# Optimization experiments

Measured on AMD Instinct MI355X. Metric: run time of the kernel, lower is better.

The kernel has to match this reference:

```python
import jax, jax.numpy as jnp
import numpy as np

B, H, W_LEN = 16, 256, 4096          # batch, height (in channels), width
R, S, L, NC = 128, 256, 16, 12       # residual ch, skip ch, n_layers, n_classes
MAX_DILATION = 256
LOOP = int(np.floor(np.log2(MAX_DILATION))) + 1  # 9 -> dilations 1..256 cycling


def conv1d(x, w, b=None, dilation=1):
    # x: [N, C, T], w: [O, I, K]
    y = jax.lax.conv_general_dilated(
        x, w, window_strides=(1,), padding='VALID',
        rhs_dilation=(dilation,), dimension_numbers=('NCH', 'OIH', 'NCH'))
    return y if b is None else y + b[None, :, None]


def setup_inputs() -> dict:
    key = jax.random.key(0)
    ks = jax.random.split(key, 8)
    f = lambda k, sh: (jax.random.normal(k, sh, jnp.float32) * 0.05)
    return {
        'input_data': jax.random.normal(ks[0], (B, H, W_LEN), jnp.float32),
        'w_in': f(ks[1], (R, H, 1)),         'b_in': jnp.zeros((R,), jnp.float32),
        'dilate_w': f(ks[2], (L, 2 * R, R, 2)), 'dilate_b': jnp.zeros((L, 2 * R), jnp.float32),
        'res_w': f(ks[3], (L - 1, R, R, 1)), 'res_b': jnp.zeros((L - 1, R), jnp.float32),
        'skip_w': f(ks[4], (L, S, R, 1)),    'skip_b': jnp.zeros((L, S), jnp.float32),
        'w_out': f(ks[5], (NC, S, 1)),
        'lin_w': f(ks[6], (NC, NC)),         'lin_b': jnp.zeros((NC,), jnp.float32),
    }


def reference(input_data, w_in, b_in, dilate_w, dilate_b, res_w, res_b,
              skip_w, skip_b, w_out, lin_w, lin_b):
    x = conv1d(input_data, w_in, b_in)   # [B, R, T]
    res_acts = None
    skip = None
    for i in range(L):
        d = 2 ** (i % LOOP)
        xi = jnp.pad(x, ((0, 0), (0, 0), (d, 0)))  # causal pad (k-1)*d, k=2
        a = conv1d(xi, dilate_w[i], dilate_b[i], dilation=d)  # [B, 2R, T]
        acts = jnp.tanh(a[:, :R]) * jax.nn.sigmoid(a[:, R:])
        if i < L - 1:
            res_acts = conv1d(acts, res_w[i], res_b[i])
        # NOTE: faithful to original: last layer reuses previous res_acts
        x = res_acts + x
        sk = conv1d(acts, skip_w[i], skip_b[i])
        skip = sk if i == 0 else skip + sk
    out = conv1d(skip, w_out)            # [B, NC, T], no bias
    out = jnp.mean(out, axis=2)          # AvgPool1d(kernel=W_LEN) + view -> [B, NC]
    return out @ lin_w.T + lin_b
```

## Files before the change

### kernel.cpp

```cpp
#include <hip/hip_runtime.h>
#include <hip/hip_bf16.h>


#define KC 32

typedef __bf16 bf16_t;
typedef __bf16 bf16x4 __attribute__((ext_vector_type(4)));
typedef __bf16 bf16x8 __attribute__((ext_vector_type(8)));
typedef float f32x16 __attribute__((ext_vector_type(16)));

__device__ __align__(16) __bf16 g_wi_dev[32768];
__device__ float g_pooled[4096];

__device__ __forceinline__ void gl_lds16(const void* g, void* l) {
    __builtin_amdgcn_global_load_lds(
        (const __attribute__((address_space(1))) unsigned int*)g,
        (__attribute__((address_space(3))) unsigned int*)l, 16, 0, 0);
}

__device__ __forceinline__ float fast_sigmoid(float x) {
    float e = __builtin_amdgcn_exp2f(-1.4426950408889634f * x);
    return __builtin_amdgcn_rcpf(1.0f + e);
}
__device__ __forceinline__ float fast_tanh(float x) {
    float e = __builtin_amdgcn_exp2f(-2.8853900817779268f * x);
    return fmaf(2.0f, __builtin_amdgcn_rcpf(1.0f + e), -1.0f);
}

__global__ __launch_bounds__(256) void prep_wg_kernel(
    const float* __restrict__ dw, bf16_t* __restrict__ wg)
{
    int idx = blockIdx.x * 256 + threadIdx.x;
    int e = idx & 7, ps = (idx >> 3) & 3, row = (idx >> 5) & 255;
    int c = (idx >> 13) & 7, layer = idx >> 16;
    int s = ps ^ ((row >> 1) & 3);
    int k = c * 32 + s * 8 + e;
    int tap = k >> 7, ch = k & 127;
    wg[idx] = (bf16_t)dw[(((size_t)layer * 256 + row) * 128 + ch) * 2 + tap];
}

__global__ __launch_bounds__(256) void prep_wr_kernel(
    const float* __restrict__ rw, bf16_t* __restrict__ wr)
{
    int idx = blockIdx.x * 256 + threadIdx.x;
    int e = idx & 7, ps = (idx >> 3) & 3, row = (idx >> 5) & 127;
    int c = (idx >> 12) & 3, layer = idx >> 14;
    int s = ps ^ ((row >> 1) & 3);
    int ch = c * 32 + s * 8 + e;
    wr[idx] = (bf16_t)rw[((size_t)layer * 128 + row) * 128 + ch];
}

__global__ __launch_bounds__(256) void prep_wi_kernel(const float* __restrict__ wi)
{
    int idx = blockIdx.x * 256 + threadIdx.x;
    int e = idx & 7, ps = (idx >> 3) & 3, row = (idx >> 5) & 127;
    int c = idx >> 12;
    int s = ps ^ ((row >> 1) & 3);
    int ch = c * 32 + s * 8 + e;
    g_wi_dev[idx] = (bf16_t)wi[(size_t)row * 256 + ch];
}

__global__ __launch_bounds__(256) void zero_misc_kernel(bf16_t* __restrict__ zeros)
{
    int idx = blockIdx.x * 256 + threadIdx.x;
    zeros[idx] = (bf16_t)0.0f;
    if (idx < 4096) g_pooled[idx] = 0.0f;
}

__global__ __launch_bounds__(256) void transpose_in(
    const float* __restrict__ input, bf16_t* __restrict__ th,
    bf16_t* __restrict__ tl, int b_off)
{
    __shared__ float Sl[64][65];
    const int tid = threadIdx.x;
    const int t0 = blockIdx.x * 64, ch0 = blockIdx.y * 64, bz = blockIdx.z;
    const int b = b_off + bz;
#pragma unroll
    for (int it = 0; it < 16; ++it) {
        int idx = it * 256 + tid;
        int t = idx & 63, ch = idx >> 6;
        Sl[ch][t] = input[((size_t)b * 256 + ch0 + ch) * 4096 + t0 + t];
    }
    __syncthreads();
#pragma unroll
    for (int it = 0; it < 16; ++it) {
        int idx = it * 256 + tid;
        int ch = idx & 63, t = idx >> 6;
        float v = Sl[ch][t];
        bf16_t hb = (bf16_t)v;
        size_t o = ((size_t)bz * 4096 + t0 + t) * 256 + ch0 + ch;
        th[o] = hb;
        tl[o] = (bf16_t)(v - (float)hb);
    }
}

__global__ __launch_bounds__(512, 4) void fused_layer(
    const bf16_t* __restrict__ xc_hi, const bf16_t* __restrict__ xc_lo,
    bf16_t* __restrict__ xn_hi, bf16_t* __restrict__ xn_lo,
    const bf16_t* __restrict__ zeros,
    const bf16_t* __restrict__ wg_l, const float* __restrict__ dbias,
    const bf16_t* __restrict__ wr_l, const float* __restrict__ rbias,
    float* __restrict__ asum_l, int d, int skipres)
{
    __shared__ __align__(16) char lds[66560];
    const int tid = threadIdx.x;
    const int wave = tid >> 6, lane = tid & 63;
    const int l31 = lane & 31, h = lane >> 5;
    const int wm = wave & 3, wn = wave >> 2;

    const int wg = blockIdx.x + 32 * blockIdx.z;
    const int xcd = wg & 7;
    const int idxin = wg >> 3;
    const int b = (xcd << 1) | (idxin >> 5);
    const int tile = idxin & 31;
    const int t0 = tile * 128;

    f32x16 acc[2][2];
#pragma unroll
    for (int m = 0; m < 2; ++m)
#pragma unroll
        for (int n = 0; n < 2; ++n) acc[m][n] = (f32x16)(0.0f);

    const int t_pos = tid >> 2;
    const int s_x = (tid & 3) ^ ((t_pos >> 1) & 3);
    const int chx = s_x << 3;

    auto stage_g = [&](int u, int sl) {
        const char* wsrc = (const char*)wg_l + (size_t)u * 16384;
        char* wdst = lds + sl * 16384;
        gl_lds16(wsrc + tid * 16, wdst + tid * 16);
        gl_lds16(wsrc + (tid + 512) * 16, wdst + (tid + 512) * 16);
        int tap = (u >> 2) & 1;
        int ch = ((u & 3) << 5) + chx;
        int tg = t0 + t_pos - (tap ? 0 : d);
        const bf16_t* sph = (tg >= 0)
            ? (xc_hi + ((size_t)b * 4096 + tg) * 128 + ch) : (zeros + ch);
        gl_lds16(sph, lds + 32768 + sl * 8192 + tid * 16);
    };

    stage_g(0, 0);
    const int swz = (l31 >> 1) & 3;
    int aoff[2][2], boff[2][2];
#pragma unroll
    for (int m = 0; m < 2; ++m)
#pragma unroll
        for (int s2 = 0; s2 < 2; ++s2)
            aoff[m][s2] = ((m ? 128 + wm * 32 : wm * 32) + l31) * 64 +
                          (((s2 * 2 + h) ^ swz) << 4);
#pragma unroll
    for (int n = 0; n < 2; ++n)
#pragma unroll
        for (int s2 = 0; s2 < 2; ++s2)
            boff[n][s2] = (wn * 64 + n * 32 + l31) * 64 + (((s2 * 2 + h) ^ swz) << 4);

    for (int u = 0; u < 8; ++u) {
        if (u < 7) {
            stage_g(u + 1, (u + 1) & 1);
            asm volatile("s_waitcnt vmcnt(3)" ::: "memory");
        } else {
            asm volatile("s_waitcnt vmcnt(0)" ::: "memory");
        }
        __builtin_amdgcn_s_barrier();

        const char* whb = lds + (u & 1) * 16384;
        const char* xhb = lds + 32768 + (u & 1) * 8192;
        bf16x8 a0[2], a1[2], b0[2], b1[2];
#pragma unroll
        for (int s2 = 0; s2 < 2; ++s2) {
            a0[s2] = *(const bf16x8*)(whb + aoff[0][s2]);
            a1[s2] = *(const bf16x8*)(whb + aoff[1][s2]);
            b0[s2] = *(const bf16x8*)(xhb + boff[0][s2]);
            b1[s2] = *(const bf16x8*)(xhb + boff[1][s2]);
        }
        __builtin_amdgcn_s_setprio(1);
#pragma unroll
        for (int s2 = 0; s2 < 2; ++s2) {
            acc[0][0] = __builtin_amdgcn_mfma_f32_32x32x16_bf16(a0[s2], b0[s2], acc[0][0], 0, 0, 0);
            acc[0][1] = __builtin_amdgcn_mfma_f32_32x32x16_bf16(a0[s2], b1[s2], acc[0][1], 0, 0, 0);
            acc[1][0] = __builtin_amdgcn_mfma_f32_32x32x16_bf16(a1[s2], b0[s2], acc[1][0], 0, 0, 0);
            acc[1][1] = __builtin_amdgcn_mfma_f32_32x32x16_bf16(a1[s2], b1[s2], acc[1][1], 0, 0, 0);
        }
        __builtin_amdgcn_s_setprio(0);
        __builtin_amdgcn_s_barrier();
    }
    __syncthreads();

    if (!skipres) {
#pragma unroll
        for (int r = 0; r < 4; ++r)
            gl_lds16((const char*)wr_l + (r * 512 + tid) * 16,
                     lds + 32768 + (r * 512 + tid) * 16);
    }

    float psum[16];
#pragma unroll
    for (int u = 0; u < 16; ++u) psum[u] = 0.0f;

#pragma unroll
    for (int n = 0; n < 2; ++n) {
        int t = wn * 64 + n * 32 + l31;
        int sw = (t & 7) << 4;
#pragma unroll
        for (int rg = 0; rg < 4; ++rg) {
            int ch0 = wm * 32 + rg * 8 + 4 * h;
            bf16x4 hv;
#pragma unroll
            for (int j = 0; j < 4; ++j) {
                int r = rg * 4 + j;
                float a1v = acc[0][n][r] + dbias[ch0 + j];
                float a2v = acc[1][n][r] + dbias[128 + ch0 + j];
                float a = fast_tanh(a1v) * fast_sigmoid(a2v);
                psum[rg * 4 + j] += a;
                hv[j] = (bf16_t)a;
            }
            int low = (t * 256 + ch0 * 2) ^ sw;
            *(bf16x4*)(lds + low) = hv;
        }
    }

#pragma unroll
    for (int u = 0; u < 16; ++u) {
        float v = psum[u];
        v += __shfl_xor(v, 1);
        v += __shfl_xor(v, 2);
        v += __shfl_xor(v, 4);
        v += __shfl_xor(v, 8);
        v += __shfl_xor(v, 16);
        psum[u] = v;
    }
    if (l31 == 0) {
        float* ps = (float*)(lds + 65536);
#pragma unroll
        for (int u = 0; u < 16; ++u) {
            int ch = wm * 32 + (u >> 2) * 8 + 4 * h + (u & 3);
            ps[wn * 128 + ch] = psum[u];
        }
    }

    asm volatile("s_waitcnt vmcnt(0) lgkmcnt(0)" ::: "memory");
    __builtin_amdgcn_s_barrier();

    if (tid < 128) {
        const float* ps = (const float*)(lds + 65536);
        asum_l[((size_t)b * 32 + tile) * 128 + tid] = ps[tid] + ps[128 + tid];
    }
    if (skipres) return;

    f32x16 accr[2];
    accr[0] = (f32x16)(0.0f);
    accr[1] = (f32x16)(0.0f);
    int tl_[2], mk_[2];
#pragma unroll
    for (int n = 0; n < 2; ++n) {
        tl_[n] = wn * 64 + n * 32 + l31;
        mk_[n] = (tl_[n] & 7) << 4;
    }

    __builtin_amdgcn_s_setprio(1);
#pragma unroll
    for (int u = 0; u < 4; ++u) {
        const char* ab = lds + 32768 + u * 8192;
        int cb = u << 6;
        bf16x8 av[2], bv[2][2];
#pragma unroll
        for (int s2 = 0; s2 < 2; ++s2) {
            av[s2] = *(const bf16x8*)(ab + (wm * 32 + l31) * 64 +
                                      (((s2 * 2 + h) ^ swz) << 4));
#pragma unroll
            for (int n = 0; n < 2; ++n) {
                int low = (cb + ((s2 * 2 + h) << 4)) ^ mk_[n];
                bv[n][s2] = *(const bf16x8*)(lds + tl_[n] * 256 + low);
            }
        }
#pragma unroll
        for (int s2 = 0; s2 < 2; ++s2) {
            accr[0] = __builtin_amdgcn_mfma_f32_32x32x16_bf16(av[s2], bv[0][s2], accr[0], 0, 0, 0);
            accr[1] = __builtin_amdgcn_mfma_f32_32x32x16_bf16(av[s2], bv[1][s2], accr[1], 0, 0, 0);
        }
    }
    __builtin_amdgcn_s_setprio(0);
    __syncthreads();

#pragma unroll
    for (int n = 0; n < 2; ++n) {
        int t = tl_[n];
        int sw = (t & 7) << 4;
#pragma unroll
        for (int rg = 0; rg < 4; ++rg) {
            int ch0 = wm * 32 + rg * 8 + 4 * h;
            bf16x4 hv, lv;
#pragma unroll
            for (int j = 0; j < 4; ++j) {
                float v = accr[n][rg * 4 + j] + rbias[ch0 + j];
                bf16_t hb = (bf16_t)v;
                hv[j] = hb;
                lv[j] = (bf16_t)(v - (float)hb);
            }
            int low = (t * 256 + ch0 * 2) ^ sw;
            *(bf16x4*)(lds + low) = hv;
            *(bf16x4*)(lds + 32768 + low) = lv;
        }
    }
    __syncthreads();

#pragma unroll
    for (int it = 0; it < 4; ++it) {
        int g = it * 512 + tid;
        int byte = g * 16;
        int t = byte >> 8;
        int off = byte & 255;
        int phys = byte ^ ((t & 7) << 4);
        bf16x8 hv = *(const bf16x8*)(lds + phys);
        bf16x8 lv = *(const bf16x8*)(lds + 32768 + phys);
        size_t gofs = ((size_t)b * 4096 + t0 + t) * 256 + off;
        bf16x8 oh = *(const bf16x8*)((const char*)xc_hi + gofs);
        bf16x8 ol = *(const bf16x8*)((const char*)xc_lo + gofs);
        bf16x8 nh, nl;
#pragma unroll
        for (int j = 0; j < 8; ++j) {
            float v = (float)hv[j] + (float)lv[j] + (float)oh[j] + (float)ol[j];
            bf16_t hb = (bf16_t)v;
            nh[j] = hb;
            nl[j] = (bf16_t)(v - (float)hb);
        }
        *(bf16x8*)((char*)xn_hi + gofs) = nh;
        *(bf16x8*)((char*)xn_lo + gofs) = nl;
    }
}

__global__ __launch_bounds__(256) void pw_mfma_in(
    const bf16_t* __restrict__ sh, const bf16_t* __restrict__ sl,
    const float* __restrict__ bias,
    bf16_t* __restrict__ xth, bf16_t* __restrict__ xtl, int b_off)
{
    __shared__ __align__(16) char lds[49152];
    const int tid = threadIdx.x;
    const int wave = tid >> 6, lane = tid & 63;
    const int l31 = lane & 31, h = lane >> 5;
    const int wm = wave & 1, wn = wave >> 1;
    const int t0 = blockIdx.x * 128;
    const int bz = blockIdx.z;
    const bf16_t* w = (const bf16_t*)g_wi_dev;

    f32x16 acc[2][2];
#pragma unroll
    for (int m = 0; m < 2; ++m)
#pragma unroll
        for (int n = 0; n < 2; ++n) acc[m][n] = (f32x16)(0.0f);

    auto stage = [&](int u, int sl_) {
        const char* wsrc = (const char*)w + (size_t)u * 8192;
        char* wdst = lds + sl_ * 8192;
        gl_lds16(wsrc + tid * 16, wdst + tid * 16);
        gl_lds16(wsrc + (tid + 256) * 16, wdst + (tid + 256) * 16);
#pragma unroll
        for (int it = 0; it < 2; ++it) {
            int row = (tid >> 2) + it * 64;
            int ps = tid & 3;
            int sx = ps ^ ((row >> 1) & 3);
            size_t gi = ((size_t)bz * 4096 + t0 + row) * 256 + u * 32 + sx * 8;
            gl_lds16(sh + gi, lds + 16384 + sl_ * 8192 + (row * 4 + ps) * 16);
            gl_lds16(sl + gi, lds + 32768 + sl_ * 8192 + (row * 4 + ps) * 16);
        }
    };

    stage(0, 0);
    const int swz = (l31 >> 1) & 3;
    int aoff[2][2], boff[2][2];
#pragma unroll
    for (int m = 0; m < 2; ++m)
#pragma unroll
        for (int s2 = 0; s2 < 2; ++s2)
            aoff[m][s2] = (wm * 64 + m * 32 + l31) * 64 + (((s2 * 2 + h) ^ swz) << 4);
#pragma unroll
    for (int n = 0; n < 2; ++n)
#pragma unroll
        for (int s2 = 0; s2 < 2; ++s2)
            boff[n][s2] = (wn * 64 + n * 32 + l31) * 64 + (((s2 * 2 + h) ^ swz) << 4);

    for (int u = 0; u < 8; ++u) {
        if (u < 7) {
            stage(u + 1, (u + 1) & 1);
            asm volatile("s_waitcnt vmcnt(6)" ::: "memory");
        } else {
            asm volatile("s_waitcnt vmcnt(0)" ::: "memory");
        }
        __builtin_amdgcn_s_barrier();

        const char* wb = lds + (u & 1) * 8192;
#pragma unroll
        for (int ph = 0; ph < 2; ++ph) {
            const char* xb = lds + (ph ? 32768 : 16384) + (u & 1) * 8192;
            bf16x8 a0[2], a1[2], b0[2], b1[2];
#pragma unroll
            for (int s2 = 0; s2 < 2; ++s2) {
                a0[s2] = *(const bf16x8*)(wb + aoff[0][s2]);
                a1[s2] = *(const bf16x8*)(wb + aoff[1][s2]);
                b0[s2] = *(const bf16x8*)(xb + boff[0][s2]);
                b1[s2] = *(const bf16x8*)(xb + boff[1][s2]);
            }
#pragma unroll
            for (int s2 = 0; s2 < 2; ++s2) {
                acc[0][0] = __builtin_amdgcn_mfma_f32_32x32x16_bf16(a0[s2], b0[s2], acc[0][0], 0, 0, 0);
                acc[0][1] = __builtin_amdgcn_mfma_f32_32x32x16_bf16(a0[s2], b1[s2], acc[0][1], 0, 0, 0);
                acc[1][0] = __builtin_amdgcn_mfma_f32_32x32x16_bf16(a1[s2], b0[s2], acc[1][0], 0, 0, 0);
                acc[1][1] = __builtin_amdgcn_mfma_f32_32x32x16_bf16(a1[s2], b1[s2], acc[1][1], 0, 0, 0);
            }
        }
        __builtin_amdgcn_s_barrier();
    }

    const int b = b_off + bz;
#pragma unroll
    for (int n = 0; n < 2; ++n) {
        int t = wn * 64 + n * 32 + l31;
        size_t trow = ((size_t)b * 4096 + t0 + t) * 128;
#pragma unroll
        for (int m = 0; m < 2; ++m) {
#pragma unroll
            for (int rg = 0; rg < 4; ++rg) {
                int ch0 = wm * 64 + m * 32 + rg * 8 + 4 * h;
                bf16x4 nh, nl;
#pragma unroll
                for (int j = 0; j < 4; ++j) {
                    float v = acc[m][n][rg * 4 + j] + bias[ch0 + j];
                    bf16_t hb = (bf16_t)v;
                    nh[j] = hb;
                    nl[j] = (bf16_t)(v - (float)hb);
                }
                *(bf16x4*)(xth + trow + ch0) = nh;
                *(bf16x4*)(xtl + trow + ch0) = nl;
            }
        }
    }
}

__global__ __launch_bounds__(256) void skip_partial(
    const float* __restrict__ asum2, const float* __restrict__ skip_w)
{
    const int i = blockIdx.x >> 4, b = blockIdx.x & 15, s = threadIdx.x;
    __shared__ float as_[128];
    if (s < 128) {
        const float* p = asum2 + ((size_t)(i * 16 + b) * 32) * 128 + s;
        float v = 0.0f;
#pragma unroll
        for (int tl2 = 0; tl2 < 32; ++tl2) v += p[tl2 * 128];
        as_[s] = v;
    }
    __syncthreads();
    const float* sw = skip_w + ((size_t)i * 256 + s) * 128;
    float t = 0.0f;
#pragma unroll 8
    for (int r = 0; r < 128; ++r) t = fmaf(sw[r], as_[r], t);
    atomicAdd(&g_pooled[b * 256 + s], t);
}

__global__ __launch_bounds__(256) void head_kernel(
    const float* __restrict__ skip_b, const float* __restrict__ w_out,
    const float* __restrict__ lin_w, const float* __restrict__ lin_b,
    float* __restrict__ out)
{
    const int b = blockIdx.x;
    const int s = threadIdx.x;
    float sb = 0.0f;
#pragma unroll
    for (int i = 0; i < 16; ++i) sb += skip_b[i * 256 + s];
    __shared__ float pl[256];
    pl[s] = g_pooled[b * 256 + s] * (1.0f / 4096.0f) + sb;
    __syncthreads();
    __shared__ float o1[12];
    if (s < 12) {
        float v = 0.0f;
        for (int q = 0; q < 256; ++q) v = fmaf(w_out[s * 256 + q], pl[q], v);
        o1[s] = v;
    }
    __syncthreads();
    if (s < 12) {
        float v = lin_b[s];
#pragma unroll
        for (int m = 0; m < 12; ++m) v = fmaf(lin_w[s * 12 + m], o1[m], v);
        out[b * 12 + s] = v;
    }
}

__global__ __launch_bounds__(256) void pw_conv_kernel(
    const float* __restrict__ src, const float* __restrict__ W,
    const float* __restrict__ bias, float* __restrict__ dst,
    int K, int accumulate)
{
    __shared__ float Wl[KC][68];
    __shared__ float Sl[KC][68];
    const int tid = threadIdx.x;
    const int t0 = blockIdx.x * 64;
    const int row0 = blockIdx.y * 64;
    const int b = blockIdx.z;
    const int i4 = (tid >> 4) * 4;
    const int j4 = (tid & 15) * 4;
    float acc[4][4];
#pragma unroll
    for (int r = 0; r < 4; ++r) {
        float bv = bias[row0 + i4 + r];
#pragma unroll
        for (int c = 0; c < 4; ++c) acc[r][c] = bv;
    }
    const float* sb = src + (size_t)b * K * 4096;
    for (int k0 = 0; k0 < K; k0 += KC) {
        __syncthreads();
#pragma unroll
        for (int it = 0; it < 8; ++it) {
            int idx = it * 256 + tid;
            int kk = idx & 31, oo = idx >> 5;
            Wl[kk][oo] = W[(size_t)(row0 + oo) * K + (k0 + kk)];
        }
#pragma unroll
        for (int it = 0; it < 8; ++it) {
            int idx = it * 256 + tid;
            int t = idx & 63, kk = idx >> 6;
            Sl[kk][t] = sb[(size_t)(k0 + kk) * 4096 + t0 + t];
        }
        __syncthreads();
#pragma unroll
        for (int kk = 0; kk < KC; ++kk) {
            float4 wv = *(const float4*)&Wl[kk][i4];
            float4 sv = *(const float4*)&Sl[kk][j4];
            float wr_[4] = {wv.x, wv.y, wv.z, wv.w};
            float sc[4] = {sv.x, sv.y, sv.z, sv.w};
#pragma unroll
            for (int r = 0; r < 4; ++r)
#pragma unroll
                for (int c = 0; c < 4; ++c)
                    acc[r][c] = fmaf(wr_[r], sc[c], acc[r][c]);
        }
    }
    float* db = dst + (size_t)b * 128 * 4096;
#pragma unroll
    for (int r = 0; r < 4; ++r) {
        float* p = db + (size_t)(row0 + i4 + r) * 4096 + t0 + j4;
        float4 v;
        if (accumulate) {
            float4 old = *(const float4*)p;
            v.x = acc[r][0] + old.x; v.y = acc[r][1] + old.y;
            v.z = acc[r][2] + old.z; v.w = acc[r][3] + old.w;
        } else {
            v.x = acc[r][0]; v.y = acc[r][1]; v.z = acc[r][2]; v.w = acc[r][3];
        }
        *(float4*)p = v;
    }
}

__global__ __launch_bounds__(256) void gated_conv_kernel(
    const float* __restrict__ x, const float* __restrict__ Wd,
    const float* __restrict__ dbias, float* __restrict__ acts, int d)
{
    __shared__ float Wt0[KC][68], Wt1[KC][68], Ws0[KC][68], Ws1[KC][68];
    __shared__ float Sc[KC][68], Sp[KC][68];
    const int tid = threadIdx.x;
    const int t0 = blockIdx.x * 64;
    const int row0 = blockIdx.y * 64;
    const int b = blockIdx.z;
    const int i4 = (tid >> 4) * 4;
    const int j4 = (tid & 15) * 4;
    float a1[4][4], a2[4][4];
#pragma unroll
    for (int r = 0; r < 4; ++r) {
        float bt = dbias[row0 + i4 + r];
        float bs = dbias[128 + row0 + i4 + r];
#pragma unroll
        for (int c = 0; c < 4; ++c) { a1[r][c] = bt; a2[r][c] = bs; }
    }
    const float* xb = x + (size_t)b * 128 * 4096;
    for (int k0 = 0; k0 < 128; k0 += KC) {
        __syncthreads();
#pragma unroll
        for (int it = 0; it < 8; ++it) {
            int idx = it * 256 + tid;
            int kk = idx & 31, oo = idx >> 5;
            float2 wt = *(const float2*)(Wd + ((size_t)(row0 + oo) * 128 + (k0 + kk)) * 2);
            float2 ws = *(const float2*)(Wd + ((size_t)(128 + row0 + oo) * 128 + (k0 + kk)) * 2);
            Wt0[kk][oo] = wt.x; Wt1[kk][oo] = wt.y;
            Ws0[kk][oo] = ws.x; Ws1[kk][oo] = ws.y;
        }
#pragma unroll
        for (int it = 0; it < 8; ++it) {
            int idx = it * 256 + tid;
            int t = idx & 63, kk = idx >> 6;
            Sc[kk][t] = xb[(size_t)(k0 + kk) * 4096 + t0 + t];
            int gt = t0 + t - d;
            Sp[kk][t] = (gt >= 0) ? xb[(size_t)(k0 + kk) * 4096 + gt] : 0.0f;
        }
        __syncthreads();
#pragma unroll
        for (int kk = 0; kk < KC; ++kk) {
            float4 xcv4 = *(const float4*)&Sc[kk][j4];
            float4 xpv4 = *(const float4*)&Sp[kk][j4];
            float4 wt0 = *(const float4*)&Wt0[kk][i4];
            float4 wt1 = *(const float4*)&Wt1[kk][i4];
            float4 ws0 = *(const float4*)&Ws0[kk][i4];
            float4 ws1 = *(const float4*)&Ws1[kk][i4];
            float xc[4] = {xcv4.x, xcv4.y, xcv4.z, xcv4.w};
            float xp[4] = {xpv4.x, xpv4.y, xpv4.z, xpv4.w};
            float t0r[4] = {wt0.x, wt0.y, wt0.z, wt0.w};
            float t1r[4] = {wt1.x, wt1.y, wt1.z, wt1.w};
            float s0r[4] = {ws0.x, ws0.y, ws0.z, ws0.w};
            float s1r[4] = {ws1.x, ws1.y, ws1.z, ws1.w};
#pragma unroll
            for (int r = 0; r < 4; ++r)
#pragma unroll
                for (int c = 0; c < 4; ++c) {
                    a1[r][c] = fmaf(t0r[r], xp[c], a1[r][c]);
                    a1[r][c] = fmaf(t1r[r], xc[c], a1[r][c]);
                    a2[r][c] = fmaf(s0r[r], xp[c], a2[r][c]);
                    a2[r][c] = fmaf(s1r[r], xc[c], a2[r][c]);
                }
        }
    }
    float* ab = acts + (size_t)b * 128 * 4096;
#pragma unroll
    for (int r = 0; r < 4; ++r) {
        float4 v;
#pragma unroll
        for (int c = 0; c < 4; ++c) {
            float th = tanhf(a1[r][c]);
            float sg = 1.0f / (1.0f + expf(-a2[r][c]));
            ((float*)&v)[c] = th * sg;
        }
        *(float4*)&ab[(size_t)(row0 + i4 + r) * 4096 + t0 + j4] = v;
    }
}

__global__ __launch_bounds__(256) void actsum_kernel(
    const float* __restrict__ acts, float* __restrict__ out)
{
    const int br = blockIdx.x;
    const float* p = acts + (size_t)br * 4096;
    float s = 0.0f;
#pragma unroll
    for (int c = 0; c < 16; ++c) s += p[c * 256 + threadIdx.x];
    __shared__ float red[256];
    red[threadIdx.x] = s;
    __syncthreads();
    for (int off = 128; off > 0; off >>= 1) {
        if (threadIdx.x < off) red[threadIdx.x] += red[threadIdx.x + off];
        __syncthreads();
    }
    if (threadIdx.x == 0) out[br] = red[0];
}

__global__ __launch_bounds__(256) void final_kernel(
    const float* __restrict__ actsum, const float* __restrict__ skip_w,
    const float* __restrict__ skip_b, const float* __restrict__ w_out,
    const float* __restrict__ lin_w, const float* __restrict__ lin_b,
    float* __restrict__ out)
{
    const int b = blockIdx.x;
    const int s = threadIdx.x;
    float acc = 0.0f;
    for (int i = 0; i < 16; ++i) {
        const float* sw = skip_w + ((size_t)i * 256 + s) * 128;
        const float* as = actsum + ((size_t)i * 16 + b) * 128;
        float t = 0.0f;
#pragma unroll 8
        for (int r = 0; r < 128; ++r) t = fmaf(sw[r], as[r], t);
        acc += t;
    }
    float sb = 0.0f;
    for (int i = 0; i < 16; ++i) sb += skip_b[i * 256 + s];
    __shared__ float pl[256];
    pl[s] = acc * (1.0f / 4096.0f) + sb;
    __syncthreads();
    __shared__ float o1[12];
    if (s < 12) {
        float v = 0.0f;
        for (int qq = 0; qq < 256; ++qq) v = fmaf(w_out[s * 256 + qq], pl[qq], v);
        o1[s] = v;
    }
    __syncthreads();
    if (s < 12) {
        float v = lin_b[s];
#pragma unroll
        for (int m = 0; m < 12; ++m) v = fmaf(lin_w[s * 12 + m], o1[m], v);
        out[b * 12 + s] = v;
    }
}

extern "C" void kernel_launch(void* const* d_in, const int* in_sizes, int n_in,
                              void* d_out, int out_size, void* d_ws, size_t ws_size,
                              hipStream_t stream)
{
    const float* input    = (const float*)d_in[0];
    const float* w_in     = (const float*)d_in[1];
    const float* b_in     = (const float*)d_in[2];
    const float* dilate_w = (const float*)d_in[3];
    const float* dilate_b = (const float*)d_in[4];
    const float* res_w    = (const float*)d_in[5];
    const float* res_b    = (const float*)d_in[6];
    const float* skip_w   = (const float*)d_in[7];
    const float* skip_b   = (const float*)d_in[8];
    const float* w_out    = (const float*)d_in[9];
    const float* lin_w    = (const float*)d_in[10];
    const float* lin_b    = (const float*)d_in[11];
    float* out = (float*)d_out;

    const size_t NEED = 77103104ULL;
    if (ws_size >= NEED) {
        char* base = (char*)d_ws;
        bf16_t* xtA_hi = (bf16_t*)(base);
        bf16_t* xtA_lo = (bf16_t*)(base + 16777216);
        bf16_t* xtB_hi = (bf16_t*)(base + 33554432);
        bf16_t* xtB_lo = (bf16_t*)(base + 50331648);
        bf16_t* wg     = (bf16_t*)(base + 67108864);
        bf16_t* wr     = (bf16_t*)(base + 69206016);
        float*  asum2  = (float*)(base + 69730304);
        bf16_t* zeros  = (bf16_t*)(base + 73924608);

        zero_misc_kernel<<<dim3(128), dim3(256), 0, stream>>>(zeros);
        prep_wg_kernel<<<dim3(4096), dim3(256), 0, stream>>>(dilate_w, wg);
        prep_wr_kernel<<<dim3(960), dim3(256), 0, stream>>>(res_w, wr);
        prep_wi_kernel<<<dim3(128), dim3(256), 0, stream>>>(w_in);

        for (int pass = 0; pass < 2; ++pass) {
            transpose_in<<<dim3(64, 4, 8), dim3(256), 0, stream>>>(
                input, xtB_hi, xtB_lo, pass * 8);
            pw_mfma_in<<<dim3(32, 1, 8), dim3(256), 0, stream>>>(
                xtB_hi, xtB_lo, b_in, xtA_hi, xtA_lo, pass * 8);
        }

        for (int i = 0; i < 16; ++i) {
            int d = 1 << (i % 9);
            const bf16_t* xc_hi = (i & 1) ? xtB_hi : xtA_hi;
            const bf16_t* xc_lo = (i & 1) ? xtB_lo : xtA_lo;
            bf16_t* xn_hi = (i & 1) ? xtA_hi : xtB_hi;
            bf16_t* xn_lo = (i & 1) ? xtA_lo : xtB_lo;
            int skipres = (i == 15) ? 1 : 0;
            fused_layer<<<dim3(32, 1, 16), dim3(512), 0, stream>>>(
                xc_hi, xc_lo, xn_hi, xn_lo, zeros,
                wg + (size_t)i * 65536, dilate_b + i * 256,
                wr + (size_t)(skipres ? 0 : i) * 16384,
                res_b + (skipres ? 0 : i) * 128,
                asum2 + (size_t)i * 65536, d, skipres);
        }
        skip_partial<<<dim3(256), dim3(256), 0, stream>>>(asum2, skip_w);
        head_kernel<<<dim3(16), dim3(256), 0, stream>>>(
            skip_b, w_out, lin_w, lin_b, out);
    } else {
        float* ws   = (float*)d_ws;
        float* x    = ws;
        float* acts = ws + 8388608;
        float* asum = ws + 16777216;
        dim3 grid(64, 2, 16), blk(256, 1, 1);
        pw_conv_kernel<<<grid, blk, 0, stream>>>(input, w_in, b_in, x, 256, 0);
        for (int i = 0; i < 16; ++i) {
            int d = 1 << (i % 9);
            gated_conv_kernel<<<grid, blk, 0, stream>>>(
                x, dilate_w + (size_t)i * 256 * 128 * 2, dilate_b + i * 256, acts, d);
            actsum_kernel<<<dim3(2048), blk, 0, stream>>>(acts, asum + i * 2048);
            if (i < 15) {
                pw_conv_kernel<<<grid, blk, 0, stream>>>(
                    acts, res_w + (size_t)i * 128 * 128, res_b + i * 128, x, 128, 1);
            }
        }
        final_kernel<<<dim3(16), blk, 0, stream>>>(
            asum, skip_w, skip_b, w_out, lin_w, lin_b, out);
    }
}
```

Measured before the change: 486.5 us.

## Drop bf16 hi/lo split residual stream and triple-buffer gated conv staging

Replaces the two-part bf16 (hi+lo) representation of the residual stream with a single bf16 tensor in the input transpose, the input pointwise conv, and each fused layer. This halves residual reads and writes and the low-part LDS staging and MFMA work in the input conv. It also moves the fused layer's weight/activation staging from double to triple buffering with deeper prefetch, which raises LDS use. The cost is lower residual precision accumulated over 16 layers, which risks exceeding the accuracy tolerance.

```diff
diff --git a/kernel.cpp b/kernel.cpp
--- a/kernel.cpp
+++ b/kernel.cpp
@@ -68,8 +68,7 @@
 }
 
 __global__ __launch_bounds__(256) void transpose_in(
-    const float* __restrict__ input, bf16_t* __restrict__ th,
-    bf16_t* __restrict__ tl, int b_off)
+    const float* __restrict__ input, bf16_t* __restrict__ th, int b_off)
 {
     __shared__ float Sl[64][65];
     const int tid = threadIdx.x;
@@ -86,23 +85,18 @@
     for (int it = 0; it < 16; ++it) {
         int idx = it * 256 + tid;
         int ch = idx & 63, t = idx >> 6;
-        float v = Sl[ch][t];
-        bf16_t hb = (bf16_t)v;
-        size_t o = ((size_t)bz * 4096 + t0 + t) * 256 + ch0 + ch;
-        th[o] = hb;
-        tl[o] = (bf16_t)(v - (float)hb);
+        th[((size_t)bz * 4096 + t0 + t) * 256 + ch0 + ch] = (bf16_t)Sl[ch][t];
     }
 }
 
 __global__ __launch_bounds__(512, 4) void fused_layer(
-    const bf16_t* __restrict__ xc_hi, const bf16_t* __restrict__ xc_lo,
-    bf16_t* __restrict__ xn_hi, bf16_t* __restrict__ xn_lo,
+    const bf16_t* __restrict__ xc, bf16_t* __restrict__ xn,
     const bf16_t* __restrict__ zeros,
     const bf16_t* __restrict__ wg_l, const float* __restrict__ dbias,
     const bf16_t* __restrict__ wr_l, const float* __restrict__ rbias,
     float* __restrict__ asum_l, int d, int skipres)
 {
-    __shared__ __align__(16) char lds[66560];
+    __shared__ __align__(16) char lds[73728];
     const int tid = threadIdx.x;
     const int wave = tid >> 6, lane = tid & 63;
     const int l31 = lane & 31, h = lane >> 5;
@@ -125,7 +119,8 @@
     const int s_x = (tid & 3) ^ ((t_pos >> 1) & 3);
     const int chx = s_x << 3;
 
-    auto stage_g = [&](int u, int sl) {
+    auto stage_g = [&](int u) {
+        int sl = u % 3;
         const char* wsrc = (const char*)wg_l + (size_t)u * 16384;
         char* wdst = lds + sl * 16384;
         gl_lds16(wsrc + tid * 16, wdst + tid * 16);
@@ -134,11 +129,12 @@
         int ch = ((u & 3) << 5) + chx;
         int tg = t0 + t_pos - (tap ? 0 : d);
         const bf16_t* sph = (tg >= 0)
-            ? (xc_hi + ((size_t)b * 4096 + tg) * 128 + ch) : (zeros + ch);
-        gl_lds16(sph, lds + 32768 + sl * 8192 + tid * 16);
+            ? (xc + ((size_t)b * 4096 + tg) * 128 + ch) : (zeros + ch);
+        gl_lds16(sph, lds + 49152 + sl * 8192 + tid * 16);
     };
 
-    stage_g(0, 0);
+    stage_g(0);
+    stage_g(1);
     const int swz = (l31 >> 1) & 3;
     int aoff[2][2], boff[2][2];
 #pragma unroll
@@ -154,16 +150,18 @@
             boff[n][s2] = (wn * 64 + n * 32 + l31) * 64 + (((s2 * 2 + h) ^ swz) << 4);
 
     for (int u = 0; u < 8; ++u) {
-        if (u < 7) {
-            stage_g(u + 1, (u + 1) & 1);
+        if (u < 6) {
+            stage_g(u + 2);
+            asm volatile("s_waitcnt vmcnt(6)" ::: "memory");
+        } else if (u < 7) {
             asm volatile("s_waitcnt vmcnt(3)" ::: "memory");
         } else {
             asm volatile("s_waitcnt vmcnt(0)" ::: "memory");
         }
         __builtin_amdgcn_s_barrier();
 
-        const char* whb = lds + (u & 1) * 16384;
-        const char* xhb = lds + 32768 + (u & 1) * 8192;
+        const char* whb = lds + (u % 3) * 16384;
+        const char* xhb = lds + 49152 + (u % 3) * 8192;
         bf16x8 a0[2], a1[2], b0[2], b1[2];
 #pragma unroll
         for (int s2 = 0; s2 < 2; ++s2) {
@@ -288,17 +286,12 @@
 #pragma unroll
         for (int rg = 0; rg < 4; ++rg) {
             int ch0 = wm * 32 + rg * 8 + 4 * h;
-            bf16x4 hv, lv;
-#pragma unroll
-            for (int j = 0; j < 4; ++j) {
-                float v = accr[n][rg * 4 + j] + rbias[ch0 + j];
-                bf16_t hb = (bf16_t)v;
-                hv[j] = hb;
-                lv[j] = (bf16_t)(v - (float)hb);
-            }
+            bf16x4 hv;
+#pragma unroll
+            for (int j = 0; j < 4; ++j)
+                hv[j] = (bf16_t)(accr[n][rg * 4 + j] + rbias[ch0 + j]);
             int low = (t * 256 + ch0 * 2) ^ sw;
             *(bf16x4*)(lds + low) = hv;
-            *(bf16x4*)(lds + 32768 + low) = lv;
         }
     }
     __syncthreads();
@@ -311,29 +304,21 @@
         int off = byte & 255;
         int phys = byte ^ ((t & 7) << 4);
         bf16x8 hv = *(const bf16x8*)(lds + phys);
-        bf16x8 lv = *(const bf16x8*)(lds + 32768 + phys);
         size_t gofs = ((size_t)b * 4096 + t0 + t) * 256 + off;
-        bf16x8 oh = *(const bf16x8*)((const char*)xc_hi + gofs);
-        bf16x8 ol = *(const bf16x8*)((const char*)xc_lo + gofs);
-        bf16x8 nh, nl;
-#pragma unroll
-        for (int j = 0; j < 8; ++j) {
-            float v = (float)hv[j] + (float)lv[j] + (float)oh[j] + (float)ol[j];
-            bf16_t hb = (bf16_t)v;
-            nh[j] = hb;
-            nl[j] = (bf16_t)(v - (float)hb);
-        }
-        *(bf16x8*)((char*)xn_hi + gofs) = nh;
-        *(bf16x8*)((char*)xn_lo + gofs) = nl;
+        bf16x8 oh = *(const bf16x8*)((const char*)xc + gofs);
+        bf16x8 nh;
+#pragma unroll
+        for (int j = 0; j < 8; ++j)
+            nh[j] = (bf16_t)((float)hv[j] + (float)oh[j]);
+        *(bf16x8*)((char*)xn + gofs) = nh;
     }
 }
 
 __global__ __launch_bounds__(256) void pw_mfma_in(
-    const bf16_t* __restrict__ sh, const bf16_t* __restrict__ sl,
-    const float* __restrict__ bias,
-    bf16_t* __restrict__ xth, bf16_t* __restrict__ xtl, int b_off)
-{
-    __shared__ __align__(16) char lds[49152];
+    const bf16_t* __restrict__ sh, const float* __restrict__ bias,
+    bf16_t* __restrict__ xth, int b_off)
+{
+    __shared__ __align__(16) char lds[32768];
     const int tid = threadIdx.x;
     const int wave = tid >> 6, lane = tid & 63;
     const int l31 = lane & 31, h = lane >> 5;
@@ -360,7 +345,6 @@
             int sx = ps ^ ((row >> 1) & 3);
             size_t gi = ((size_t)bz * 4096 + t0 + row) * 256 + u * 32 + sx * 8;
             gl_lds16(sh + gi, lds + 16384 + sl_ * 8192 + (row * 4 + ps) * 16);
-            gl_lds16(sl + gi, lds + 32768 + sl_ * 8192 + (row * 4 + ps) * 16);
         }
     };
 
@@ -381,31 +365,28 @@
     for (int u = 0; u < 8; ++u) {
         if (u < 7) {
             stage(u + 1, (u + 1) & 1);
-            asm volatile("s_waitcnt vmcnt(6)" ::: "memory");
+            asm volatile("s_waitcnt vmcnt(4)" ::: "memory");
         } else {
             asm volatile("s_waitcnt vmcnt(0)" ::: "memory");
         }
         __builtin_amdgcn_s_barrier();
 
         const char* wb = lds + (u & 1) * 8192;
-#pragma unroll
-        for (int ph = 0; ph < 2; ++ph) {
-            const char* xb = lds + (ph ? 32768 : 16384) + (u & 1) * 8192;
-            bf16x8 a0[2], a1[2], b0[2], b1[2];
-#pragma unroll
-            for (int s2 = 0; s2 < 2; ++s2) {
-                a0[s2] = *(const bf16x8*)(wb + aoff[0][s2]);
-                a1[s2] = *(const bf16x8*)(wb + aoff[1][s2]);
-                b0[s2] = *(const bf16x8*)(xb + boff[0][s2]);
-                b1[s2] = *(const bf16x8*)(xb + boff[1][s2]);
-            }
-#pragma unroll
-            for (int s2 = 0; s2 < 2; ++s2) {
-                acc[0][0] = __builtin_amdgcn_mfma_f32_32x32x16_bf16(a0[s2], b0[s2], acc[0][0], 0, 0, 0);
-                acc[0][1] = __builtin_amdgcn_mfma_f32_32x32x16_bf16(a0[s2], b1[s2], acc[0][1], 0, 0, 0);
-                acc[1][0] = __builtin_amdgcn_mfma_f32_32x32x16_bf16(a1[s2], b0[s2], acc[1][0], 0, 0, 0);
-                acc[1][1] = __builtin_amdgcn_mfma_f32_32x32x16_bf16(a1[s2], b1[s2], acc[1][1], 0, 0, 0);
-            }
+        const char* xb = lds + 16384 + (u & 1) * 8192;
+        bf16x8 a0[2], a1[2], b0[2], b1[2];
+#pragma unroll
+        for (int s2 = 0; s2 < 2; ++s2) {
+            a0[s2] = *(const bf16x8*)(wb + aoff[0][s2]);
+            a1[s2] = *(const bf16x8*)(wb + aoff[1][s2]);
+            b0[s2] = *(const bf16x8*)(xb + boff[0][s2]);
+            b1[s2] = *(const bf16x8*)(xb + boff[1][s2]);
+        }
+#pragma unroll
+        for (int s2 = 0; s2 < 2; ++s2) {
+            acc[0][0] = __builtin_amdgcn_mfma_f32_32x32x16_bf16(a0[s2], b0[s2], acc[0][0], 0, 0, 0);
+            acc[0][1] = __builtin_amdgcn_mfma_f32_32x32x16_bf16(a0[s2], b1[s2], acc[0][1], 0, 0, 0);
+            acc[1][0] = __builtin_amdgcn_mfma_f32_32x32x16_bf16(a1[s2], b0[s2], acc[1][0], 0, 0, 0);
+            acc[1][1] = __builtin_amdgcn_mfma_f32_32x32x16_bf16(a1[s2], b1[s2], acc[1][1], 0, 0, 0);
         }
         __builtin_amdgcn_s_barrier();
     }
@@ -420,16 +401,11 @@
 #pragma unroll
             for (int rg = 0; rg < 4; ++rg) {
                 int ch0 = wm * 64 + m * 32 + rg * 8 + 4 * h;
-                bf16x4 nh, nl;
-#pragma unroll
-                for (int j = 0; j < 4; ++j) {
-                    float v = acc[m][n][rg * 4 + j] + bias[ch0 + j];
-                    bf16_t hb = (bf16_t)v;
-                    nh[j] = hb;
-                    nl[j] = (bf16_t)(v - (float)hb);
-                }
+                bf16x4 nh;
+#pragma unroll
+                for (int j = 0; j < 4; ++j)
+                    nh[j] = (bf16_t)(acc[m][n][rg * 4 + j] + bias[ch0 + j]);
                 *(bf16x4*)(xth + trow + ch0) = nh;
-                *(bf16x4*)(xtl + trow + ch0) = nl;
             }
         }
     }
@@ -704,14 +680,12 @@
     const size_t NEED = 77103104ULL;
     if (ws_size >= NEED) {
         char* base = (char*)d_ws;
-        bf16_t* xtA_hi = (bf16_t*)(base);
-        bf16_t* xtA_lo = (bf16_t*)(base + 16777216);
-        bf16_t* xtB_hi = (bf16_t*)(base + 33554432);
-        bf16_t* xtB_lo = (bf16_t*)(base + 50331648);
-        bf16_t* wg     = (bf16_t*)(base + 67108864);
-        bf16_t* wr     = (bf16_t*)(base + 69206016);
-        float*  asum2  = (float*)(base + 69730304);
-        bf16_t* zeros  = (bf16_t*)(base + 73924608);
+        bf16_t* xtA   = (bf16_t*)(base);
+        bf16_t* xtB   = (bf16_t*)(base + 16777216);
+        bf16_t* wg    = (bf16_t*)(base + 33554432);
+        bf16_t* wr    = (bf16_t*)(base + 35651584);
+        float*  asum2 = (float*)(base + 36175872);
+        bf16_t* zeros = (bf16_t*)(base + 40370176);
 
         zero_misc_kernel<<<dim3(128), dim3(256), 0, stream>>>(zeros);
         prep_wg_kernel<<<dim3(4096), dim3(256), 0, stream>>>(dilate_w, wg);
@@ -720,20 +694,18 @@
 
         for (int pass = 0; pass < 2; ++pass) {
             transpose_in<<<dim3(64, 4, 8), dim3(256), 0, stream>>>(
-                input, xtB_hi, xtB_lo, pass * 8);
+                input, xtB, pass * 8);
             pw_mfma_in<<<dim3(32, 1, 8), dim3(256), 0, stream>>>(
-                xtB_hi, xtB_lo, b_in, xtA_hi, xtA_lo, pass * 8);
+                xtB, b_in, xtA, pass * 8);
         }
 
         for (int i = 0; i < 16; ++i) {
             int d = 1 << (i % 9);
-            const bf16_t* xc_hi = (i & 1) ? xtB_hi : xtA_hi;
-            const bf16_t* xc_lo = (i & 1) ? xtB_lo : xtA_lo;
-            bf16_t* xn_hi = (i & 1) ? xtA_hi : xtB_hi;
-            bf16_t* xn_lo = (i & 1) ? xtA_lo : xtB_lo;
+            const bf16_t* xc = (i & 1) ? xtB : xtA;
+            bf16_t* xn = (i & 1) ? xtA : xtB;
             int skipres = (i == 15) ? 1 : 0;
             fused_layer<<<dim3(32, 1, 16), dim3(512), 0, stream>>>(
-                xc_hi, xc_lo, xn_hi, xn_lo, zeros,
+                xc, xn, zeros,
                 wg + (size_t)i * 65536, dilate_b + i * 256,
                 wr + (size_t)(skipres ? 0 : i) * 16384,
                 res_b + (skipres ? 0 : i) * 128,
```

Result: faster. 392.0 us (median of 2 runs) (-19.4%).
